# Optimization experiments

Hardware: AMD Instinct MI355X
Metric: run time of the kernel (lower is better)

## Reference

```python
import jax, jax.numpy as jnp
import numpy as np

DIM = 1024
HEADS = 16
HEAD_DIM = DIM // HEADS
THRESH = 0.29514
SHARP = 15.0
LN_EPS = 1e-5
NORM_EPS = 1e-12


def setup_inputs() -> dict:
    key = jax.random.key(0)
    ks = jax.random.split(key, 8)
    s = 1.0 / np.sqrt(DIM)
    sg = 1.0 / np.sqrt(HEAD_DIM)
    return {
        "x": jax.random.normal(ks[0], (2, 2048, DIM), dtype=jnp.float32),
        "Wq": jax.random.uniform(ks[1], (DIM, DIM), jnp.float32, -s, s),
        "Wk": jax.random.uniform(ks[2], (DIM, DIM), jnp.float32, -s, s),
        "Wv": jax.random.uniform(ks[3], (DIM, DIM), jnp.float32, -s, s),
        "gq": jax.random.uniform(ks[4], (HEAD_DIM,), jnp.float32, -sg, sg),
        "gk": jax.random.uniform(ks[5], (HEAD_DIM,), jnp.float32, -sg, sg),
        "Wo": jax.random.uniform(ks[6], (DIM, DIM), jnp.float32, -s, s),
        "bo": jax.random.uniform(ks[7], (DIM,), jnp.float32, -s, s),
        "ln_w": jnp.ones((DIM,), jnp.float32),
        "ln_b": jnp.zeros((DIM,), jnp.float32),
    }


def _l2norm(t):
    # F.normalize: t / max(||t||_2, eps)
    n = jnp.sqrt(jnp.sum(t * t, axis=-1, keepdims=True))
    return t / jnp.maximum(n, NORM_EPS)


def reference(x, Wq, Wk, Wv, gq, gk, Wo, bo, ln_w, ln_b):
    B, T, D = x.shape
    # LayerNorm over last dim
    mu = jnp.mean(x, axis=-1, keepdims=True)
    var = jnp.mean((x - mu) ** 2, axis=-1, keepdims=True)
    x_norm = (x - mu) / jnp.sqrt(var + LN_EPS) * ln_w + ln_b

    def split_heads(t):  # [B,T,D] -> [B,H,T,hd]
        return t.reshape(B, T, HEADS, HEAD_DIM).transpose(0, 2, 1, 3)

    q = _l2norm(split_heads(x_norm @ Wq))
    k = _l2norm(split_heads(x_norm @ Wk))
    v = split_heads(x @ Wv)  # note: v uses un-normalized x, as in source

    align = jnp.einsum("bhtd,bhsd->bhts", q, k)  # cosine alignment
    resonance = jax.nn.sigmoid((align - THRESH) * SHARP)
    gate_q = jnp.einsum("bhtd,d->bht", q, gq)
    gate_k = jnp.einsum("bhsd,d->bhs", k, gk)
    modulation = resonance * gate_q[..., :, None] * gate_k[..., None, :]
    collapse = jnp.einsum("bhts,bhsd->bhtd", modulation, v)
    collapse = collapse.transpose(0, 2, 1, 3).reshape(B, T, D)
    return collapse @ Wo + bo
```

## Files before the change

### kernel.cpp

```cpp
#include <hip/hip_runtime.h>
#include <math.h>

#define DIM 1024
#define T_SEQ 2048
#define NBATCH 2
#define HEADS 16
#define HD 64
#define NTOK 4096
#define THRESH 0.29514f
#define SHARP 15.0f
#define LOG2E 1.4426950408889634f

typedef __attribute__((ext_vector_type(8))) short bf16x8;
typedef __attribute__((ext_vector_type(4))) float f32x4;

__device__ __forceinline__ unsigned short f2b(float f) {
    unsigned int u = __float_as_uint(f);
    unsigned int r = (u + 0x7FFFu + ((u >> 16) & 1u)) >> 16;
    return (unsigned short)r;
}
__device__ __forceinline__ float b2f(unsigned short u) {
    return __uint_as_float(((unsigned int)u) << 16);
}

__device__ __forceinline__ void async_cp16(const unsigned short* g, unsigned short* l) {
    __builtin_amdgcn_global_load_lds(
        (const __attribute__((address_space(1))) unsigned int*)g,
        (__attribute__((address_space(3))) unsigned int*)l, 16, 0, 0);
}

__global__ __launch_bounds__(256) void ln_xnorm_kernel(
    const float* __restrict__ x, const float* __restrict__ lnw, const float* __restrict__ lnb,
    unsigned short* __restrict__ xnb, unsigned short* __restrict__ xb) {
    int row = blockIdx.x * 4 + (threadIdx.x >> 6);
    int lane = threadIdx.x & 63;
    const float4* xr = (const float4*)(x + (size_t)row * DIM);
    float4 v[4];
    float s = 0.f, ss = 0.f;
#pragma unroll
    for (int i = 0; i < 4; i++) {
        v[i] = xr[lane + i * 64];
        s += v[i].x + v[i].y + v[i].z + v[i].w;
        ss += v[i].x * v[i].x + v[i].y * v[i].y + v[i].z * v[i].z + v[i].w * v[i].w;
    }
#pragma unroll
    for (int off = 32; off; off >>= 1) {
        s += __shfl_xor(s, off);
        ss += __shfl_xor(ss, off);
    }
    float m = s * (1.f / DIM);
    float rstd = rsqrtf(ss * (1.f / DIM) - m * m + 1e-5f);
#pragma unroll
    for (int i = 0; i < 4; i++) {
        int e = (lane + i * 64) * 4;
        float4 lw = *(const float4*)&lnw[e];
        float4 lb = *(const float4*)&lnb[e];
        ushort4 un, ur;
        un.x = f2b((v[i].x - m) * rstd * lw.x + lb.x);
        un.y = f2b((v[i].y - m) * rstd * lw.y + lb.y);
        un.z = f2b((v[i].z - m) * rstd * lw.z + lb.z);
        un.w = f2b((v[i].w - m) * rstd * lw.w + lb.w);
        ur.x = f2b(v[i].x); ur.y = f2b(v[i].y); ur.z = f2b(v[i].z); ur.w = f2b(v[i].w);
        *(ushort4*)&xnb[(size_t)row * DIM + e] = un;
        *(ushort4*)&xb[(size_t)row * DIM + e] = ur;
    }
}

__global__ __launch_bounds__(256) void wtrans_kernel(
    const float* __restrict__ W0, const float* __restrict__ W1,
    const float* __restrict__ W2, const float* __restrict__ W3,
    unsigned short* __restrict__ T0, unsigned short* __restrict__ T1,
    unsigned short* __restrict__ T2, unsigned short* __restrict__ T3) {
    __shared__ float tile[64][65];
    const int z = blockIdx.z;
    const float* W = (z == 0) ? W0 : (z == 1) ? W1 : (z == 2) ? W2 : W3;
    unsigned short* T = (z == 0) ? T0 : (z == 1) ? T1 : (z == 2) ? T2 : T3;
    const int k0 = blockIdx.x * 64, n0 = blockIdx.y * 64;
    const int r = threadIdx.x >> 3;
    const int c = (threadIdx.x & 7) * 8;
#pragma unroll
    for (int half = 0; half < 2; half++) {
        int rr = r + half * 32;
        float4 a = *(const float4*)&W[(size_t)(k0 + rr) * DIM + n0 + c];
        float4 b = *(const float4*)&W[(size_t)(k0 + rr) * DIM + n0 + c + 4];
        tile[rr][c + 0] = a.x; tile[rr][c + 1] = a.y; tile[rr][c + 2] = a.z; tile[rr][c + 3] = a.w;
        tile[rr][c + 4] = b.x; tile[rr][c + 5] = b.y; tile[rr][c + 6] = b.z; tile[rr][c + 7] = b.w;
    }
    __syncthreads();
#pragma unroll
    for (int half = 0; half < 2; half++) {
        int dd = r + half * 32;
        bf16x8 o;
#pragma unroll
        for (int j = 0; j < 8; j++) o[j] = (short)f2b(tile[c + j][dd]);
        *(bf16x8*)&T[(size_t)(n0 + dd) * DIM + k0 + c] = o;
    }
}

template <int MODE>
__global__ __launch_bounds__(256) void gemm_mfma_kernel(
    const unsigned short* __restrict__ A0, const unsigned short* __restrict__ A2,
    const unsigned short* __restrict__ Bt0, const unsigned short* __restrict__ Bt1,
    const unsigned short* __restrict__ Bt2, const float* __restrict__ bias,
    const float* __restrict__ gq, const float* __restrict__ gk,
    unsigned short* __restrict__ Oq, unsigned short* __restrict__ Ok,
    unsigned short* __restrict__ Ov, float* __restrict__ gq_t, float* __restrict__ gk_t,
    float* __restrict__ Oout) {
    __shared__ __align__(16) unsigned short As[128 * 32];
    __shared__ __align__(16) unsigned short Bs[128 * 32];
    const int tid = threadIdx.x;
    const int lane = tid & 63, w = tid >> 6;
    const int l16 = lane & 15, quad = lane >> 4;
    const int wm = w >> 1, wn = w & 1;
    const int m0 = blockIdx.x * 128, n0 = blockIdx.y * 128;
    const unsigned short* A;
    const unsigned short* Bt;
    int z = 0;
    if constexpr (MODE == 0) {
        z = blockIdx.z;
        A = (z == 2) ? A2 : A0;
        Bt = (z == 0) ? Bt0 : (z == 1) ? Bt1 : Bt2;
    } else {
        A = A0;
        Bt = Bt0;
    }
    f32x4 acc[4][4] = {};
    const int kswz = (l16 >> 1) & 3;

    for (int k0 = 0; k0 < DIM; k0 += 32) {
        __syncthreads();
#pragma unroll
        for (int i = 0; i < 2; i++) {
            int linear = i * 256 + tid;
            int m = linear >> 2, kgp = linear & 3;
            int kgl = kgp ^ ((m >> 1) & 3);
            async_cp16(A + (size_t)(m0 + m) * DIM + k0 + kgl * 8, As + linear * 8);
            async_cp16(Bt + (size_t)(n0 + m) * DIM + k0 + kgl * 8, Bs + linear * 8);
        }
        __syncthreads();
        bf16x8 af[4], bfr[4];
#pragma unroll
        for (int t = 0; t < 4; t++) {
            int ma = wm * 64 + t * 16 + l16;
            af[t] = *(const bf16x8*)(As + ma * 32 + ((quad ^ kswz) * 8));
            int nb = wn * 64 + t * 16 + l16;
            bfr[t] = *(const bf16x8*)(Bs + nb * 32 + ((quad ^ kswz) * 8));
        }
#pragma unroll
        for (int mt = 0; mt < 4; mt++)
#pragma unroll
            for (int nt = 0; nt < 4; nt++)
                acc[mt][nt] =
                    __builtin_amdgcn_mfma_f32_16x16x32_bf16(af[mt], bfr[nt], acc[mt][nt], 0, 0, 0);
    }

    if constexpr (MODE == 0) {
        const int h = (n0 + wn * 64) >> 6;
        if (z <= 1) {
            const float* gvec = (z == 0) ? gq : gk;
            float* gate = (z == 0) ? gq_t : gk_t;
            unsigned short* O = (z == 0) ? Oq : Ok;
            float gv[4];
#pragma unroll
            for (int nt = 0; nt < 4; nt++) gv[nt] = gvec[nt * 16 + l16];
#pragma unroll
            for (int mt = 0; mt < 4; mt++) {
#pragma unroll
                for (int r = 0; r < 4; r++) {
                    float ss = 0.f;
#pragma unroll
                    for (int nt = 0; nt < 4; nt++) ss += acc[mt][nt][r] * acc[mt][nt][r];
#pragma unroll
                    for (int msk = 1; msk < 16; msk <<= 1) ss += __shfl_xor(ss, msk);
                    float rn = __builtin_amdgcn_rcpf(fmaxf(sqrtf(ss), 1e-12f));
                    float vn[4], gg = 0.f;
#pragma unroll
                    for (int nt = 0; nt < 4; nt++) {
                        vn[nt] = acc[mt][nt][r] * rn;
                        gg += vn[nt] * gv[nt];
                    }
#pragma unroll
                    for (int msk = 1; msk < 16; msk <<= 1) gg += __shfl_xor(gg, msk);
                    int tok = m0 + wm * 64 + mt * 16 + quad * 4 + r;
                    int b = tok >> 11, t = tok & 2047;
                    size_t rowbase = ((size_t)(b * HEADS + h) * T_SEQ + t) * HD;
#pragma unroll
                    for (int nt = 0; nt < 4; nt++) O[rowbase + nt * 16 + l16] = f2b(vn[nt]);
                    if (l16 == 0) gate[(b * HEADS + h) * T_SEQ + t] = gg;
                }
            }
        } else {
#pragma unroll
            for (int mt = 0; mt < 4; mt++) {
#pragma unroll
                for (int r = 0; r < 4; r++) {
                    int tok = m0 + wm * 64 + mt * 16 + quad * 4 + r;
                    int b = tok >> 11, t = tok & 2047;
                    size_t rowbase = ((size_t)(b * HEADS + h) * T_SEQ + t) * HD;
#pragma unroll
                    for (int nt = 0; nt < 4; nt++)
                        Ov[rowbase + nt * 16 + l16] = f2b(acc[mt][nt][r]);
                }
            }
        }
    } else {
        float bias_r[4];
#pragma unroll
        for (int nt = 0; nt < 4; nt++) bias_r[nt] = bias[n0 + wn * 64 + nt * 16 + l16];
#pragma unroll
        for (int mt = 0; mt < 4; mt++) {
#pragma unroll
            for (int r = 0; r < 4; r++) {
                int tok = m0 + wm * 64 + mt * 16 + quad * 4 + r;
#pragma unroll
                for (int nt = 0; nt < 4; nt++) {
                    int n = n0 + wn * 64 + nt * 16 + l16;
                    Oout[(size_t)tok * DIM + n] = acc[mt][nt][r] + bias_r[nt];
                }
            }
        }
    }
}

__global__ __launch_bounds__(256) void vtrans_kernel(const unsigned short* __restrict__ Vn,
                                                     const float* __restrict__ gk_t,
                                                     unsigned short* __restrict__ Vt) {
    __shared__ float tile[64][65];
    const int bh = blockIdx.y;
    const int t0 = blockIdx.x * 64;
    const int r = threadIdx.x >> 3;
    const int c = (threadIdx.x & 7) * 8;
    const unsigned short* src = Vn + (size_t)bh * T_SEQ * HD;
#pragma unroll
    for (int half = 0; half < 2; half++) {
        int rr = r + half * 32;
        float gkv = gk_t[bh * T_SEQ + t0 + rr];
        bf16x8 v = *(const bf16x8*)(src + (size_t)(t0 + rr) * HD + c);
#pragma unroll
        for (int j = 0; j < 8; j++) tile[rr][c + j] = b2f((unsigned short)v[j]) * gkv;
    }
    __syncthreads();
    unsigned short* dst = Vt + (size_t)bh * HD * T_SEQ;
#pragma unroll
    for (int half = 0; half < 2; half++) {
        int dd = r + half * 32;
        bf16x8 o;
#pragma unroll
        for (int j = 0; j < 8; j++) o[j] = (short)f2b(tile[c + j][dd]);
        *(bf16x8*)(dst + (size_t)dd * T_SEQ + t0 + c) = o;
    }
}

__global__ __launch_bounds__(256) void attn_mfma_kernel(
    const unsigned short* __restrict__ Qn, const unsigned short* __restrict__ Kn,
    const unsigned short* __restrict__ Vt, const float* __restrict__ gateq,
    unsigned short* __restrict__ collb) {
    __shared__ __align__(16) unsigned short Ks[2][64 * 72];
    __shared__ __align__(16) unsigned short VtL[2][64 * 72];
    __shared__ __align__(16) unsigned short Sw[4][32 * 72];
    const int tid = threadIdx.x;
    const int lane = tid & 63, w = tid >> 6;
    const int quad = lane >> 4, l16 = lane & 15;
    const int t0 = blockIdx.x * 128;
    const int h = blockIdx.y, b = blockIdx.z;
    const int bh = b * HEADS + h;
    const size_t base = (size_t)bh * T_SEQ * HD;
    constexpr float K1 = -SHARP * LOG2E;
    constexpr float K0 = THRESH * SHARP * LOG2E;

    bf16x8 fq[2][2];
#pragma unroll
    for (int mt = 0; mt < 2; mt++) {
        const unsigned short* qrow = Qn + base + (size_t)(t0 + w * 32 + mt * 16 + l16) * HD;
        fq[mt][0] = *(const bf16x8*)(qrow + quad * 8);
        fq[mt][1] = *(const bf16x8*)(qrow + 32 + quad * 8);
    }

    f32x4 oacc[4][2] = {};
    unsigned short* myS = Sw[w];
    const int sr = tid >> 3;
    const int sc = (tid & 7) * 8;

    bf16x8 kr0, kr1, vr0, vr1;
    kr0 = *(const bf16x8*)(Kn + base + (size_t)sr * HD + sc);
    kr1 = *(const bf16x8*)(Kn + base + (size_t)(sr + 32) * HD + sc);
    vr0 = *(const bf16x8*)(Vt + base + (size_t)sr * T_SEQ + sc);
    vr1 = *(const bf16x8*)(Vt + base + (size_t)(sr + 32) * T_SEQ + sc);
    *(bf16x8*)(Ks[0] + sr * 72 + sc) = kr0;
    *(bf16x8*)(Ks[0] + (sr + 32) * 72 + sc) = kr1;
    *(bf16x8*)(VtL[0] + sr * 72 + sc) = vr0;
    *(bf16x8*)(VtL[0] + (sr + 32) * 72 + sc) = vr1;
    __syncthreads();

    for (int i = 0; i < T_SEQ / 64; i++) {
        const unsigned short* ksb = Ks[i & 1];
        const unsigned short* vtb = VtL[i & 1];
        const bool more = (i + 1) < (T_SEQ / 64);
        if (more) {
            int s0n = (i + 1) * 64;
            kr0 = *(const bf16x8*)(Kn + base + (size_t)(s0n + sr) * HD + sc);
            kr1 = *(const bf16x8*)(Kn + base + (size_t)(s0n + sr + 32) * HD + sc);
            vr0 = *(const bf16x8*)(Vt + base + (size_t)sr * T_SEQ + s0n + sc);
            vr1 = *(const bf16x8*)(Vt + base + (size_t)(sr + 32) * T_SEQ + s0n + sc);
        }

#pragma unroll
        for (int ct = 0; ct < 4; ct++) {
            bf16x8 fk0 = *(const bf16x8*)(ksb + (ct * 16 + l16) * 72 + quad * 8);
            bf16x8 fk1 = *(const bf16x8*)(ksb + (ct * 16 + l16) * 72 + 32 + quad * 8);
#pragma unroll
            for (int mt = 0; mt < 2; mt++) {
                f32x4 sacc = {0.f, 0.f, 0.f, 0.f};
                sacc = __builtin_amdgcn_mfma_f32_16x16x32_bf16(fk0, fq[mt][0], sacc, 0, 0, 0);
                sacc = __builtin_amdgcn_mfma_f32_16x16x32_bf16(fk1, fq[mt][1], sacc, 0, 0, 0);
                ushort4 p;
                p.x = f2b(__builtin_amdgcn_rcpf(1.f + __builtin_amdgcn_exp2f(fmaf(sacc[0], K1, K0))));
                p.y = f2b(__builtin_amdgcn_rcpf(1.f + __builtin_amdgcn_exp2f(fmaf(sacc[1], K1, K0))));
                p.z = f2b(__builtin_amdgcn_rcpf(1.f + __builtin_amdgcn_exp2f(fmaf(sacc[2], K1, K0))));
                p.w = f2b(__builtin_amdgcn_rcpf(1.f + __builtin_amdgcn_exp2f(fmaf(sacc[3], K1, K0))));
                *(ushort4*)(myS + (mt * 16 + l16) * 72 + ct * 16 + quad * 4) = p;
            }
        }

#pragma unroll
        for (int kh = 0; kh < 2; kh++) {
            bf16x8 fs0 = *(const bf16x8*)(myS + (0 * 16 + l16) * 72 + kh * 32 + quad * 8);
            bf16x8 fs1 = *(const bf16x8*)(myS + (1 * 16 + l16) * 72 + kh * 32 + quad * 8);
#pragma unroll
            for (int dt = 0; dt < 4; dt++) {
                bf16x8 fv = *(const bf16x8*)(vtb + (dt * 16 + l16) * 72 + kh * 32 + quad * 8);
                oacc[dt][0] = __builtin_amdgcn_mfma_f32_16x16x32_bf16(fv, fs0, oacc[dt][0], 0, 0, 0);
                oacc[dt][1] = __builtin_amdgcn_mfma_f32_16x16x32_bf16(fv, fs1, oacc[dt][1], 0, 0, 0);
            }
        }

        if (more) {
            unsigned short* ksn = Ks[(i + 1) & 1];
            unsigned short* vtn = VtL[(i + 1) & 1];
            *(bf16x8*)(ksn + sr * 72 + sc) = kr0;
            *(bf16x8*)(ksn + (sr + 32) * 72 + sc) = kr1;
            *(bf16x8*)(vtn + sr * 72 + sc) = vr0;
            *(bf16x8*)(vtn + (sr + 32) * 72 + sc) = vr1;
        }
        __syncthreads();
    }

#pragma unroll
    for (int mt = 0; mt < 2; mt++) {
        int t = t0 + w * 32 + mt * 16 + l16;
        float gq_v = gateq[bh * T_SEQ + t];
        unsigned short* dst = collb + ((size_t)b * T_SEQ + t) * DIM + h * HD;
#pragma unroll
        for (int dt = 0; dt < 4; dt++) {
            ushort4 o;
            o.x = f2b(oacc[dt][mt][0] * gq_v);
            o.y = f2b(oacc[dt][mt][1] * gq_v);
            o.z = f2b(oacc[dt][mt][2] * gq_v);
            o.w = f2b(oacc[dt][mt][3] * gq_v);
            *(ushort4*)(dst + dt * 16 + quad * 4) = o;
        }
    }
}

extern "C" void kernel_launch(void* const* d_in, const int* in_sizes, int n_in,
                              void* d_out, int out_size, void* d_ws, size_t ws_size,
                              hipStream_t stream) {
    const float* x = (const float*)d_in[0];
    const float* Wq = (const float*)d_in[1];
    const float* Wk = (const float*)d_in[2];
    const float* Wv = (const float*)d_in[3];
    const float* gq = (const float*)d_in[4];
    const float* gk = (const float*)d_in[5];
    const float* Wo = (const float*)d_in[6];
    const float* bo = (const float*)d_in[7];
    const float* lnw = (const float*)d_in[8];
    const float* lnb = (const float*)d_in[9];
    float* out = (float*)d_out;

    unsigned short* ws = (unsigned short*)d_ws;
    unsigned short* xnb = ws;
    unsigned short* xb = xnb + (size_t)NTOK * DIM;
    unsigned short* Wqt = xb + (size_t)NTOK * DIM;
    unsigned short* Wkt = Wqt + (size_t)DIM * DIM;
    unsigned short* Wvt = Wkt + (size_t)DIM * DIM;
    unsigned short* Wot = Wvt + (size_t)DIM * DIM;
    unsigned short* Q16 = Wot + (size_t)DIM * DIM;
    unsigned short* K16 = Q16 + (size_t)NTOK * DIM;
    unsigned short* Vn = K16 + (size_t)NTOK * DIM;
    float* gq_t = (float*)(Vn + (size_t)NTOK * DIM);
    float* gk_t = gq_t + NBATCH * HEADS * T_SEQ;
    unsigned short* Vt = xnb;
    unsigned short* collb = xb;

    ln_xnorm_kernel<<<NTOK / 4, 256, 0, stream>>>(x, lnw, lnb, xnb, xb);
    wtrans_kernel<<<dim3(16, 16, 4), 256, 0, stream>>>(Wq, Wk, Wv, Wo, Wqt, Wkt, Wvt, Wot);
    gemm_mfma_kernel<0><<<dim3(NTOK / 128, DIM / 128, 3), 256, 0, stream>>>(
        xnb, xb, Wqt, Wkt, Wvt, nullptr, gq, gk, Q16, K16, Vn, gq_t, gk_t, nullptr);
    vtrans_kernel<<<dim3(T_SEQ / 64, NBATCH * HEADS), 256, 0, stream>>>(Vn, gk_t, Vt);
    attn_mfma_kernel<<<dim3(T_SEQ / 128, HEADS, NBATCH), 256, 0, stream>>>(
        Q16, K16, Vt, gq_t, collb);
    gemm_mfma_kernel<1><<<dim3(NTOK / 128, DIM / 128, 1), 256, 0, stream>>>(
        collb, nullptr, Wot, nullptr, nullptr, bo, nullptr, nullptr, nullptr, nullptr, nullptr,
        nullptr, nullptr, out);
}
```

Measured before the change: 236.6 us.

## Keep sigmoid scores in registers via permlane swap and stage K/V with async LDS loads

The attention kernel stops round-tripping the sigmoid score tile through shared memory. It repacks the MFMA output into the B-operand layout in registers using v_permlane16_swap, with a runtime probe to pick the lane ordering. K/V staging moves from register prefetch plus LDS store to direct global-to-LDS async copies into an unpadded, XOR-swizzled layout. This cuts LDS traffic and frees shared memory for occupancy. The cost is extra register pressure, and async-copy completion now relies only on the barrier.

```diff
diff --git a/kernel.cpp b/kernel.cpp
--- a/kernel.cpp
+++ b/kernel.cpp
@@ -13,6 +13,7 @@
 
 typedef __attribute__((ext_vector_type(8))) short bf16x8;
 typedef __attribute__((ext_vector_type(4))) float f32x4;
+typedef __attribute__((ext_vector_type(4))) unsigned int u32x4;
 
 __device__ __forceinline__ unsigned short f2b(float f) {
     unsigned int u = __float_as_uint(f);
@@ -255,9 +256,8 @@
     const unsigned short* __restrict__ Qn, const unsigned short* __restrict__ Kn,
     const unsigned short* __restrict__ Vt, const float* __restrict__ gateq,
     unsigned short* __restrict__ collb) {
-    __shared__ __align__(16) unsigned short Ks[2][64 * 72];
-    __shared__ __align__(16) unsigned short VtL[2][64 * 72];
-    __shared__ __align__(16) unsigned short Sw[4][32 * 72];
+    __shared__ __align__(16) unsigned short Ks[2][64 * 64];
+    __shared__ __align__(16) unsigned short VtL[2][64 * 64];
     const int tid = threadIdx.x;
     const int lane = tid & 63, w = tid >> 6;
     const int quad = lane >> 4, l16 = lane & 15;
@@ -268,6 +268,10 @@
     constexpr float K1 = -SHARP * LOG2E;
     constexpr float K0 = THRESH * SHARP * LOG2E;
 
+    int det0 = quad, det1 = quad + 4;
+    asm("v_permlane16_swap_b32 %0, %1" : "+v"(det0), "+v"(det1));
+    const bool flagA = (__builtin_amdgcn_readfirstlane(det0) == 0);
+
     bf16x8 fq[2][2];
 #pragma unroll
     for (int mt = 0; mt < 2; mt++) {
@@ -277,70 +281,74 @@
     }
 
     f32x4 oacc[4][2] = {};
-    unsigned short* myS = Sw[w];
-    const int sr = tid >> 3;
-    const int sc = (tid & 7) * 8;
-
-    bf16x8 kr0, kr1, vr0, vr1;
-    kr0 = *(const bf16x8*)(Kn + base + (size_t)sr * HD + sc);
-    kr1 = *(const bf16x8*)(Kn + base + (size_t)(sr + 32) * HD + sc);
-    vr0 = *(const bf16x8*)(Vt + base + (size_t)sr * T_SEQ + sc);
-    vr1 = *(const bf16x8*)(Vt + base + (size_t)(sr + 32) * T_SEQ + sc);
-    *(bf16x8*)(Ks[0] + sr * 72 + sc) = kr0;
-    *(bf16x8*)(Ks[0] + (sr + 32) * 72 + sc) = kr1;
-    *(bf16x8*)(VtL[0] + sr * 72 + sc) = vr0;
-    *(bf16x8*)(VtL[0] + (sr + 32) * 72 + sc) = vr1;
+    const int srow = tid >> 3;
+    const int sgp = tid & 7;
+    const int swz = l16 & 7;
+
+    auto stage_chunk = [&](int buf, int s0) {
+#pragma unroll
+        for (int half = 0; half < 2; half++) {
+            int row = srow + half * 32;
+            int g = sgp ^ (row & 7);
+            unsigned short* ldst = &Ks[buf][0] + row * 64 + sgp * 8;
+            async_cp16(Kn + base + (size_t)(s0 + row) * HD + g * 8, ldst);
+            unsigned short* ldsv = &VtL[buf][0] + row * 64 + sgp * 8;
+            async_cp16(Vt + base + (size_t)row * T_SEQ + s0 + g * 8, ldsv);
+        }
+    };
+
+    stage_chunk(0, 0);
     __syncthreads();
 
     for (int i = 0; i < T_SEQ / 64; i++) {
-        const unsigned short* ksb = Ks[i & 1];
-        const unsigned short* vtb = VtL[i & 1];
-        const bool more = (i + 1) < (T_SEQ / 64);
-        if (more) {
-            int s0n = (i + 1) * 64;
-            kr0 = *(const bf16x8*)(Kn + base + (size_t)(s0n + sr) * HD + sc);
-            kr1 = *(const bf16x8*)(Kn + base + (size_t)(s0n + sr + 32) * HD + sc);
-            vr0 = *(const bf16x8*)(Vt + base + (size_t)sr * T_SEQ + s0n + sc);
-            vr1 = *(const bf16x8*)(Vt + base + (size_t)(sr + 32) * T_SEQ + s0n + sc);
-        }
-
+        if (i + 1 < T_SEQ / 64) stage_chunk((i + 1) & 1, (i + 1) * 64);
+        const unsigned short* ksb = &Ks[i & 1][0];
+        const unsigned short* vtb = &VtL[i & 1][0];
+
+        unsigned int p[2][4][2];
 #pragma unroll
         for (int ct = 0; ct < 4; ct++) {
-            bf16x8 fk0 = *(const bf16x8*)(ksb + (ct * 16 + l16) * 72 + quad * 8);
-            bf16x8 fk1 = *(const bf16x8*)(ksb + (ct * 16 + l16) * 72 + 32 + quad * 8);
+            const unsigned short* krow = ksb + (ct * 16 + l16) * 64;
+            bf16x8 fk0 = *(const bf16x8*)(krow + (quad ^ swz) * 8);
+            bf16x8 fk1 = *(const bf16x8*)(krow + ((quad + 4) ^ swz) * 8);
 #pragma unroll
             for (int mt = 0; mt < 2; mt++) {
                 f32x4 sacc = {0.f, 0.f, 0.f, 0.f};
                 sacc = __builtin_amdgcn_mfma_f32_16x16x32_bf16(fk0, fq[mt][0], sacc, 0, 0, 0);
                 sacc = __builtin_amdgcn_mfma_f32_16x16x32_bf16(fk1, fq[mt][1], sacc, 0, 0, 0);
-                ushort4 p;
-                p.x = f2b(__builtin_amdgcn_rcpf(1.f + __builtin_amdgcn_exp2f(fmaf(sacc[0], K1, K0))));
-                p.y = f2b(__builtin_amdgcn_rcpf(1.f + __builtin_amdgcn_exp2f(fmaf(sacc[1], K1, K0))));
-                p.z = f2b(__builtin_amdgcn_rcpf(1.f + __builtin_amdgcn_exp2f(fmaf(sacc[2], K1, K0))));
-                p.w = f2b(__builtin_amdgcn_rcpf(1.f + __builtin_amdgcn_exp2f(fmaf(sacc[3], K1, K0))));
-                *(ushort4*)(myS + (mt * 16 + l16) * 72 + ct * 16 + quad * 4) = p;
+                float w0 = __builtin_amdgcn_rcpf(1.f + __builtin_amdgcn_exp2f(fmaf(sacc[0], K1, K0)));
+                float w1 = __builtin_amdgcn_rcpf(1.f + __builtin_amdgcn_exp2f(fmaf(sacc[1], K1, K0)));
+                float w2 = __builtin_amdgcn_rcpf(1.f + __builtin_amdgcn_exp2f(fmaf(sacc[2], K1, K0)));
+                float w3 = __builtin_amdgcn_rcpf(1.f + __builtin_amdgcn_exp2f(fmaf(sacc[3], K1, K0)));
+                p[mt][ct][0] = (unsigned int)f2b(w0) | ((unsigned int)f2b(w1) << 16);
+                p[mt][ct][1] = (unsigned int)f2b(w2) | ((unsigned int)f2b(w3) << 16);
             }
         }
 
 #pragma unroll
         for (int kh = 0; kh < 2; kh++) {
-            bf16x8 fs0 = *(const bf16x8*)(myS + (0 * 16 + l16) * 72 + kh * 32 + quad * 8);
-            bf16x8 fs1 = *(const bf16x8*)(myS + (1 * 16 + l16) * 72 + kh * 32 + quad * 8);
-#pragma unroll
-            for (int dt = 0; dt < 4; dt++) {
-                bf16x8 fv = *(const bf16x8*)(vtb + (dt * 16 + l16) * 72 + kh * 32 + quad * 8);
-                oacc[dt][0] = __builtin_amdgcn_mfma_f32_16x16x32_bf16(fv, fs0, oacc[dt][0], 0, 0, 0);
-                oacc[dt][1] = __builtin_amdgcn_mfma_f32_16x16x32_bf16(fv, fs1, oacc[dt][1], 0, 0, 0);
+            int gv = (4 * kh + 2 * (quad & 1) + (quad >> 1)) ^ swz;
+            bf16x8 fv[4];
+#pragma unroll
+            for (int dt = 0; dt < 4; dt++)
+                fv[dt] = *(const bf16x8*)(vtb + (dt * 16 + l16) * 64 + gv * 8);
+#pragma unroll
+            for (int mt = 0; mt < 2; mt++) {
+                unsigned int aL = p[mt][2 * kh][0], aH = p[mt][2 * kh][1];
+                unsigned int bL = p[mt][2 * kh + 1][0], bH = p[mt][2 * kh + 1][1];
+                asm("v_permlane16_swap_b32 %0, %1" : "+v"(aL), "+v"(bL));
+                asm("v_permlane16_swap_b32 %0, %1" : "+v"(aH), "+v"(bH));
+                u32x4 bt;
+                bt.x = flagA ? aL : bL;
+                bt.y = flagA ? aH : bH;
+                bt.z = flagA ? bL : aL;
+                bt.w = flagA ? bH : aH;
+                bf16x8 fs = __builtin_bit_cast(bf16x8, bt);
+#pragma unroll
+                for (int dt = 0; dt < 4; dt++)
+                    oacc[dt][mt] =
+                        __builtin_amdgcn_mfma_f32_16x16x32_bf16(fv[dt], fs, oacc[dt][mt], 0, 0, 0);
             }
-        }
-
-        if (more) {
-            unsigned short* ksn = Ks[(i + 1) & 1];
-            unsigned short* vtn = VtL[(i + 1) & 1];
-            *(bf16x8*)(ksn + sr * 72 + sc) = kr0;
-            *(bf16x8*)(ksn + (sr + 32) * 72 + sc) = kr1;
-            *(bf16x8*)(vtn + sr * 72 + sc) = vr0;
-            *(bf16x8*)(vtn + (sr + 32) * 72 + sc) = vr1;
         }
         __syncthreads();
     }
```

Result: no change. 237.8 us (+0.5%).
